# Kernel tuning notes

Measured on AMD Instinct MI355X. Metric: run time of the kernel, lower is better.

Reference implementation:

```python
import jax, jax.numpy as jnp
import numpy as np

B = 8192        # number of drug-cell pairs (graphs)
NPG = 32        # nodes per graph
EPG = 64        # directed edges per graph
N = B * NPG     # total nodes
E = B * EPG     # total edges
CELL = 908      # cell_inp_dim
BN_EPS = 1e-5


def _bn(x):
    # BatchNorm1d in training mode with gamma=1, beta=0 (fresh init), biased var
    m = x.mean(0)
    v = x.var(0)
    return (x - m) * jax.lax.rsqrt(v + BN_EPS)


def _lin_params(k, fan_in, fan_out):
    kw, _ = jax.random.split(k)
    w = jax.random.normal(kw, (fan_in, fan_out), jnp.float32) / np.sqrt(fan_in)
    b = jnp.zeros((fan_out,), jnp.float32)
    return w, b


_DIMS = [("ce_1", CELL, 516), ("ce_2", 516, 256), ("ce_3", 256, 128),
         ("g1_1", 9, 128), ("g1_2", 128, 128),
         ("g2_1", 128, 128), ("g2_2", 128, 128),
         ("d_1", 128, 128), ("d_2", 128, 128),
         ("f_1", 256, 128), ("f_2", 128, 64), ("f_3", 64, 1)]


def setup_inputs() -> dict:
    key = jax.random.key(0)
    ks = jax.random.split(key, 4 + len(_DIMS))
    inp = {}
    inp["cell"] = jax.random.normal(ks[0], (B, CELL), jnp.float32)
    inp["drug_x"] = jax.random.normal(ks[1], (N, 9), jnp.float32)
    g = jnp.arange(E) // EPG  # graph id per edge
    src = g * NPG + jax.random.randint(ks[2], (E,), 0, NPG)
    dst = g * NPG + jax.random.randint(ks[3], (E,), 0, NPG)
    inp["drug_edge_index"] = jnp.stack([src, dst]).astype(jnp.int32)
    inp["drug_batch"] = (jnp.arange(N) // NPG).astype(jnp.int32)
    for i, (nm, a, b) in enumerate(_DIMS):
        w, bb = _lin_params(ks[4 + i], a, b)
        inp[nm + "_w"] = w
        inp[nm + "_b"] = bb
    return inp


def _forward(cell, drug_x, src, dst, batch,
             ce_1_w, ce_1_b, ce_2_w, ce_2_b, ce_3_w, ce_3_b,
             g1_1_w, g1_1_b, g1_2_w, g1_2_b,
             g2_1_w, g2_1_b, g2_2_w, g2_2_b,
             d_1_w, d_1_b, d_2_w, d_2_b,
             f_1_w, f_1_b, f_2_w, f_2_b, f_3_w, f_3_b):
    # cell_emb branch (dropout = identity in eval/reference)
    c = jax.nn.relu(_bn(cell @ ce_1_w + ce_1_b))
    c = jax.nn.relu(_bn(c @ ce_2_w + ce_2_b))
    c = jax.nn.relu(_bn(c @ ce_3_w + ce_3_b))

    # GINConv 1: h = MLP((1+eps)*x + sum_{j in N(i)} x_j), eps=0
    agg = jax.ops.segment_sum(drug_x[src], dst, num_segments=N)
    h = drug_x + agg
    h = jax.nn.relu(_bn(h @ g1_1_w + g1_1_b)) @ g1_2_w + g1_2_b  # inner MLP: Lin-BN-ReLU-Lin
    h = _bn(jax.nn.relu(h))  # outer ReLU then BN (per Sequential order)

    # GINConv 2
    agg = jax.ops.segment_sum(h[src], dst, num_segments=N)
    h = h + agg
    h = jax.nn.relu(_bn(h @ g2_1_w + g2_1_b)) @ g2_2_w + g2_2_b
    h = _bn(jax.nn.relu(h))

    # global max pool over nodes of each graph -> [B, 128]
    p = jax.ops.segment_max(h, batch, num_segments=B)

    d = jax.nn.relu(_bn(p @ d_1_w + d_1_b))
    d = jax.nn.relu(d @ d_2_w + d_2_b)

    z = jnp.concatenate([c, d], axis=-1)  # [B, 256]
    z = jax.nn.elu(_bn(z @ f_1_w + f_1_b))
    z = jax.nn.elu(_bn(z @ f_2_w + f_2_b))
    y = (z @ f_3_w + f_3_b).reshape(B)
    return y


def reference(cell, drug_x, drug_edge_index, drug_batch,
              ce_1_w, ce_1_b, ce_2_w, ce_2_b, ce_3_w, ce_3_b,
              g1_1_w, g1_1_b, g1_2_w, g1_2_b,
              g2_1_w, g2_1_b, g2_2_w, g2_2_b,
              d_1_w, d_1_b, d_2_w, d_2_b,
              f_1_w, f_1_b, f_2_w, f_2_b, f_3_w, f_3_b):
    src, dst = drug_edge_index[0], drug_edge_index[1]
    return _forward(cell, drug_x, src, dst, drug_batch,
                    ce_1_w, ce_1_b, ce_2_w, ce_2_b, ce_3_w, ce_3_b,
                    g1_1_w, g1_1_b, g1_2_w, g1_2_b,
                    g2_1_w, g2_1_b, g2_2_w, g2_2_b,
                    d_1_w, d_1_b, d_2_w, d_2_b,
                    f_1_w, f_1_b, f_2_w, f_2_b, f_3_w, f_3_b)
```

## Files before the change

kernel.cpp:

```cpp
#include <hip/hip_runtime.h>
#include <hip/hip_bf16.h>
#include <math.h>

#define BGRAPH 8192
#define NPG 32
#define EPG 64
#define NNODE (BGRAPH * NPG)
#define NEDGE (BGRAPH * EPG)
#define CELLD 908
#define BN_EPS 1e-5f
#define ABF_STR 1024
#define C1_STR 640
#define HBS 136

typedef __attribute__((ext_vector_type(8))) short bf16x8;
typedef __attribute__((ext_vector_type(4))) float f32x4;
typedef __attribute__((ext_vector_type(4))) unsigned short us4;
typedef __attribute__((ext_vector_type(8))) unsigned short us8;

__device__ __forceinline__ unsigned short f2bf(float f)
{
    unsigned int u = __float_as_uint(f);
    u = (u + 0x7FFFu + ((u >> 16) & 1u)) >> 16;
    return (unsigned short)u;
}

__device__ __forceinline__ bf16x8 quant8(const float v[8])
{
    union { bf16x8 b; unsigned short u[8]; } fr;
    #pragma unroll
    for (int j = 0; j < 8; ++j) fr.u[j] = f2bf(v[j]);
    return fr.b;
}

__device__ __forceinline__ void bf2f8(bf16x8 b, float v[8])
{
    union { bf16x8 bb; unsigned short u[8]; } x; x.bb = b;
    #pragma unroll
    for (int j = 0; j < 8; ++j) v[j] = __uint_as_float((unsigned)x.u[j] << 16);
}

__device__ __forceinline__ float apply_in(float v, int mode, float mn, float iv)
{
    if (mode == 1)      { v = (v - mn) * iv; v = fmaxf(v, 0.f); }
    else if (mode == 2) { v = (v - mn) * iv; v = (v > 0.f) ? v : expm1f(v); }
    else if (mode == 3) { v = fmaxf(v, 0.f); v = (v - mn) * iv; }
    return v;
}

struct TransArgs {
    const float* w[11];
    unsigned short* wt[11];
    int K[11], N[11], ntN[11];
    int off[12];
};
struct TransSmem { float t[64][65]; };

__device__ void dev_transpose(TransSmem* sm, int b, const TransArgs& a)
{
    int tid = threadIdx.x;
    int s = 0;
    while (s < 10 && b >= a.off[s + 1]) ++s;
    int t0 = b - a.off[s];
    int K = a.K[s], N = a.N[s], ntn = a.ntN[s];
    int kt = t0 / ntn, nt = t0 - kt * ntn;
    int k0 = kt * 64, n0 = nt * 64;
    const float* w = a.w[s];
    unsigned short* wt = a.wt[s];
    int c = tid & 63, rg = tid >> 6;
    #pragma unroll
    for (int i = 0; i < 16; ++i) {
        int rr = rg * 16 + i;
        int k = k0 + rr, n = n0 + c;
        sm->t[c][rr] = (k < K && n < N) ? w[(size_t)k * N + n] : 0.f;
    }
    __syncthreads();
    #pragma unroll
    for (int i = 0; i < 16; ++i) {
        int rr = rg * 16 + i;
        int n = n0 + rr, k = k0 + c;
        if (n < N && k < K) wt[(size_t)n * K + k] = f2bf(sm->t[rr][c]);
    }
}

struct SetupArgs {
    float* zb; int zTotal; int zBlocks;
    const int* src; const int* dst; int* row_start; int* col_idx;
};
struct SetupSmem { int cnt[4][32]; int fill[4][32]; int rsl[4][33]; };

__device__ void dev_setup(SetupSmem* sm, int b, const SetupArgs& a)
{
    int tid = threadIdx.x;
    if (b < a.zBlocks) {
        int i = b * 256 + tid;
        if (i < a.zTotal) a.zb[i] = 0.f;
        return;
    }
    b -= a.zBlocks;
    int gl = tid >> 6, e = tid & 63;
    int g = b * 4 + gl;
    if (e < 32) { sm->cnt[gl][e] = 0; sm->fill[gl][e] = 0; }
    __syncthreads();
    int s = a.src[g * EPG + e] - g * NPG;
    int d = a.dst[g * EPG + e] - g * NPG;
    atomicAdd(&sm->cnt[gl][d], 1);
    __syncthreads();
    if (e == 0) {
        int acc = 0;
        for (int i = 0; i < 32; ++i) { sm->rsl[gl][i] = acc; acc += sm->cnt[gl][i]; }
        sm->rsl[gl][32] = acc;
    }
    __syncthreads();
    int pos = sm->rsl[gl][d] + atomicAdd(&sm->fill[gl][d], 1);
    a.col_idx[g * EPG + pos] = s;
    if (e < 33) a.row_start[g * 33 + e] = sm->rsl[gl][e];
}

__device__ void dev_quant_cell(int bid, const float* __restrict__ cell,
                               unsigned short* __restrict__ abf)
{
    int i = bid * 256 + threadIdx.x;
    int row = i / (ABF_STR / 4), c4 = i - row * (ABF_STR / 4);
    int k = c4 * 4;
    us4 w = (us4){0, 0, 0, 0};
    if (k < CELLD) {
        float4 f = *(const float4*)&cell[(size_t)row * CELLD + k];
        w = (us4){ f2bf(f.x), f2bf(f.y), f2bf(f.z), f2bf(f.w) };
    }
    *(us4*)&abf[(size_t)row * ABF_STR + k] = w;
}

__device__ void dev_quant_c1(int bid, const float* __restrict__ c1,
                             const float* __restrict__ stats, float inv_sM,
                             unsigned short* __restrict__ out)
{
    int i = bid * 256 + threadIdx.x;
    int row = i / (C1_STR / 4), c4 = i - row * (C1_STR / 4);
    int k = c4 * 4;
    us4 w = (us4){0, 0, 0, 0};
    if (k < 516) {
        float4 f = *(const float4*)&c1[(size_t)row * 516 + k];
        float v[4] = {f.x, f.y, f.z, f.w};
        #pragma unroll
        for (int j = 0; j < 4; ++j) {
            float s = stats[k + j], ss = stats[516 + k + j];
            float mn = s * inv_sM;
            float iv = rsqrtf(ss * inv_sM - mn * mn + BN_EPS);
            v[j] = fmaxf((v[j] - mn) * iv, 0.f);
        }
        w = (us4){ f2bf(v[0]), f2bf(v[1]), f2bf(v[2]), f2bf(v[3]) };
    }
    *(us4*)&out[(size_t)row * C1_STR + k] = w;
}

__device__ void dev_reduce(int bid, const float* __restrict__ part, int nrows,
                           int nt, float* __restrict__ out)
{
    int c = threadIdx.x;
    int per = nrows >> 6;
    int r0 = bid * per;
    bool isq = (c >= 128);
    int cc = isq ? c - 128 : c;
    if (cc >= nt) return;
    float s = 0.f;
    for (int r = 0; r < per; ++r) s += part[(size_t)(r0 + r) * 256 + c];
    unsafeAtomicAdd(&out[(isq ? nt : 0) + cc], s);
}

struct S1Smem {
    unsigned short h[4 * 32 * HBS];
    unsigned char ubuf[4096];
    int rs[4][36];
    int ci[4][64];
};

__device__ void dev_gin_s1(S1Smem* sm, int bid,
                           const float* __restrict__ drug_x,
                           const int* __restrict__ row_start,
                           const int* __restrict__ col_idx,
                           const unsigned short* __restrict__ W11,
                           const float* __restrict__ b11,
                           unsigned short* uout, float* __restrict__ part)
{
    unsigned short* w11l = (unsigned short*)sm->ubuf;
    float* red = (float*)sm->ubuf;

    int tid  = threadIdx.x;
    int wave = tid >> 6;
    int lane = tid & 63;
    int quad = lane >> 4;
    int l16  = lane & 15;
    int g0   = bid * 4;
    unsigned short* hw = sm->h + wave * (32 * HBS);
    float* xw = (float*)hw;

    for (int i = tid; i < 128 * 16; i += 256) {
        int n = i >> 4, k = i & 15;
        w11l[i] = (k < 9) ? W11[n * 9 + k] : (unsigned short)0;
    }
    if (tid < 132) {
        int gl = tid / 33, idx = tid - gl * 33;
        sm->rs[gl][idx] = row_start[(g0 + gl) * 33 + idx];
    }
    {
        int gl = tid >> 6, e = tid & 63;
        sm->ci[gl][e] = col_idx[(g0 + gl) * EPG + e];
    }
    {
        const float* xg = drug_x + (size_t)(g0 + wave) * 32 * 9;
        for (int i = lane; i < 32 * 16; i += 64) {
            int rr = i >> 4, c = i & 15;
            xw[i] = (c < 9) ? xg[rr * 9 + c] : 0.f;
        }
    }
    __syncthreads();

    f32x4 acc[2][8];
    #pragma unroll
    for (int i = 0; i < 2; ++i)
        #pragma unroll
        for (int j = 0; j < 8; ++j)
            acc[i][j] = (f32x4){0.f, 0.f, 0.f, 0.f};

    {
        bf16x8 af[2];
        #pragma unroll
        for (int mt = 0; mt < 2; ++mt) {
            int rowl = mt * 16 + l16;
            float v[8] = {0, 0, 0, 0, 0, 0, 0, 0};
            if (quad < 2) {
                float4 lo = *(const float4*)&xw[rowl * 16 + quad * 8];
                float4 hi = *(const float4*)&xw[rowl * 16 + quad * 8 + 4];
                v[0] = lo.x; v[1] = lo.y; v[2] = lo.z; v[3] = lo.w;
                v[4] = hi.x; v[5] = hi.y; v[6] = hi.z; v[7] = hi.w;
                int e0 = sm->rs[wave][rowl], e1 = sm->rs[wave][rowl + 1];
                for (int e = e0; e < e1; ++e) {
                    int sr = sm->ci[wave][e];
                    float4 l2 = *(const float4*)&xw[sr * 16 + quad * 8];
                    float4 h2 = *(const float4*)&xw[sr * 16 + quad * 8 + 4];
                    v[0] += l2.x; v[1] += l2.y; v[2] += l2.z; v[3] += l2.w;
                    v[4] += h2.x; v[5] += h2.y; v[6] += h2.z; v[7] += h2.w;
                }
            }
            af[mt] = quant8(v);
        }
        #pragma unroll
        for (int nt = 0; nt < 8; ++nt) {
            bf16x8 b;
            if (quad < 2) b = *(const bf16x8*)(const void*)&w11l[(nt * 16 + l16) * 16 + quad * 8];
            else { float z[8] = {0,0,0,0,0,0,0,0}; b = quant8(z); }
            acc[0][nt] = __builtin_amdgcn_mfma_f32_16x16x32_bf16(af[0], b, acc[0][nt], 0, 0, 0);
            acc[1][nt] = __builtin_amdgcn_mfma_f32_16x16x32_bf16(af[1], b, acc[1][nt], 0, 0, 0);
        }
    }

    float ls[8], lq[8];
    unsigned short* ub = uout + (size_t)(g0 + wave) * 32 * 128;
    #pragma unroll
    for (int nt = 0; nt < 8; ++nt) {
        int col = nt * 16 + l16;
        float bv = b11[col];
        float s0 = 0.f, q0 = 0.f;
        #pragma unroll
        for (int mt = 0; mt < 2; ++mt) {
            int rb = mt * 16 + quad * 4;
            #pragma unroll
            for (int r = 0; r < 4; ++r) {
                float u = acc[mt][nt][r] + bv;
                ub[(size_t)(rb + r) * 128 + col] = f2bf(u);
                s0 += u; q0 += u * u;
            }
        }
        ls[nt] = s0; lq[nt] = q0;
    }
    __syncthreads();
    #pragma unroll
    for (int nt = 0; nt < 8; ++nt) {
        float s = ls[nt], q = lq[nt];
        s += __shfl_xor(s, 16); q += __shfl_xor(q, 16);
        s += __shfl_xor(s, 32); q += __shfl_xor(q, 32);
        if (quad == 0) {
            int col = nt * 16 + l16;
            red[(wave * 2 + 0) * 128 + col] = s;
            red[(wave * 2 + 1) * 128 + col] = q;
        }
    }
    __syncthreads();
    if (tid < 128) {
        float s = red[0 * 128 + tid] + red[2 * 128 + tid] + red[4 * 128 + tid] + red[6 * 128 + tid];
        float q = red[1 * 128 + tid] + red[3 * 128 + tid] + red[5 * 128 + tid] + red[7 * 128 + tid];
        part[(size_t)bid * 256 + tid] = s;
        part[(size_t)bid * 256 + 128 + tid] = q;
    }
}

struct S3fSmem {
    unsigned short wsl[128 * 136];
    float pmv[256];
    int rs[2][33];
    int ci[2][64];
};

__device__ void dev_gin_s3f(S3fSmem* sm, int bid,
                            const unsigned short* __restrict__ uin,
                            const int* __restrict__ row_start,
                            const int* __restrict__ col_idx,
                            const unsigned short* __restrict__ Wt,
                            const float* __restrict__ bias,
                            const float* __restrict__ in_stats, float inv_sM,
                            unsigned short* __restrict__ uout,
                            float* __restrict__ part)
{
    float* zt = (float*)sm->wsl;

    int tid  = threadIdx.x;
    int wave = tid >> 6;
    int lane = tid & 63;
    int quad = lane >> 4;
    int l16  = lane & 15;
    int g0   = bid * 2;
    int row0 = bid * 64;

    if (tid < 128) {
        float s = in_stats[tid], ss = in_stats[128 + tid];
        float mn = s * inv_sM;
        sm->pmv[tid] = mn;
        sm->pmv[128 + tid] = rsqrtf(ss * inv_sM - mn * mn + BN_EPS);
    }
    if (tid < 66) {
        int gl = tid / 33, idx = tid - gl * 33;
        sm->rs[gl][idx] = row_start[(g0 + gl) * 33 + idx];
    }
    if (tid >= 128) {
        int t = tid - 128;
        sm->ci[t >> 6][t & 63] = col_idx[(g0 + (t >> 6)) * EPG + (t & 63)];
    }
    for (int i = tid; i < 128 * 32; i += 256) {
        int n = i >> 5, k = (i & 31) * 4;
        *(us4*)&sm->wsl[n * 136 + k] = *(const us4*)&Wt[(size_t)n * 128 + k];
    }
    __syncthreads();

    bf16x8 afrag[4];
    {
        const unsigned short* ap = uin + (size_t)(row0 + wave * 16 + l16) * 128;
        #pragma unroll
        for (int ks = 0; ks < 4; ++ks) {
            int kb = ks * 32 + quad * 8;
            float v[8];
            bf2f8(*(const bf16x8*)(const void*)&ap[kb], v);
            #pragma unroll
            for (int j = 0; j < 8; ++j)
                v[j] = (fmaxf(v[j], 0.f) - sm->pmv[kb + j]) * sm->pmv[128 + kb + j];
            afrag[ks] = quant8(v);
        }
    }

    f32x4 acc[8];
    #pragma unroll
    for (int j = 0; j < 8; ++j) acc[j] = (f32x4){0.f, 0.f, 0.f, 0.f};
    #pragma unroll
    for (int ks = 0; ks < 4; ++ks) {
        int kb = ks * 32 + quad * 8;
        #pragma unroll
        for (int nt = 0; nt < 8; ++nt) {
            bf16x8 b = *(const bf16x8*)(const void*)&sm->wsl[(nt * 16 + l16) * 136 + kb];
            acc[nt] = __builtin_amdgcn_mfma_f32_16x16x32_bf16(afrag[ks], b, acc[nt], 0, 0, 0);
        }
    }
    __syncthreads();

    #pragma unroll
    for (int nt = 0; nt < 8; ++nt) {
        int col = nt * 16 + l16;
        #pragma unroll
        for (int r = 0; r < 4; ++r)
            zt[(wave * 16 + quad * 4 + r) * 132 + col] = acc[nt][r];
    }
    __syncthreads();

    float sv[4] = {0.f, 0.f, 0.f, 0.f}, qv[4] = {0.f, 0.f, 0.f, 0.f};
    {
        int c4  = (tid & 31) * 4;
        int rg  = tid >> 5;
        int hh  = rg >> 2;
        int rb0 = (rg & 3) * 8;
        float4 bv = *(const float4*)&bias[c4];
        unsigned short* ub = uout + (size_t)row0 * 128;
        for (int rr = 0; rr < 8; ++rr) {
            int r = rb0 + rr;
            int lr = hh * 32 + r;
            float4 val = *(const float4*)&zt[lr * 132 + c4];
            int e0 = sm->rs[hh][r], e1 = sm->rs[hh][r + 1];
            for (int e = e0; e < e1; ++e) {
                float4 zz = *(const float4*)&zt[(hh * 32 + sm->ci[hh][e]) * 132 + c4];
                val.x += zz.x; val.y += zz.y; val.z += zz.z; val.w += zz.w;
            }
            float u0 = val.x + bv.x, u1 = val.y + bv.y;
            float u2 = val.z + bv.z, u3 = val.w + bv.w;
            *(us4*)&ub[(size_t)lr * 128 + c4] =
                (us4){ f2bf(u0), f2bf(u1), f2bf(u2), f2bf(u3) };
            sv[0] += u0; sv[1] += u1; sv[2] += u2; sv[3] += u3;
            qv[0] += u0 * u0; qv[1] += u1 * u1; qv[2] += u2 * u2; qv[3] += u3 * u3;
        }
    }
    __syncthreads();
    {
        int c4 = (tid & 31) * 4, rg = tid >> 5;
        #pragma unroll
        for (int j = 0; j < 4; ++j) {
            zt[rg * 128 + c4 + j] = sv[j];
            zt[1024 + rg * 128 + c4 + j] = qv[j];
        }
    }
    __syncthreads();
    if (tid < 128) {
        float s = 0.f, q = 0.f;
        #pragma unroll
        for (int rg = 0; rg < 8; ++rg) {
            s += zt[rg * 128 + tid];
            q += zt[1024 + rg * 128 + tid];
        }
        part[(size_t)bid * 256 + tid] = s;
        part[(size_t)bid * 256 + 128 + tid] = q;
    }
}

struct LinSmem {
    unsigned short Ws_l[128 * 136];
    float pmv[256];
    float red[4][2][128];
};

template<int DO_POOL>
__device__ void dev_gin_lin(LinSmem* sm, int bid,
                            const unsigned short* __restrict__ uin,
                            const unsigned short* __restrict__ Wt,
                            const float* __restrict__ bias,
                            const float* __restrict__ in_stats, float inv_sM,
                            unsigned short* uout,
                            float* __restrict__ part,
                            float* __restrict__ pool_out)
{
    int tid  = threadIdx.x;
    int wave = tid >> 6;
    int lane = tid & 63;
    int quad = lane >> 4;
    int l16  = lane & 15;
    int row0 = bid * 64;

    for (int i = tid; i < 128 * 32; i += 256) {
        int n = i >> 5, k = (i & 31) * 4;
        *(us4*)&sm->Ws_l[n * 136 + k] = *(const us4*)&Wt[(size_t)n * 128 + k];
    }
    if (tid < 128) {
        float s = in_stats[tid], ss = in_stats[128 + tid];
        float mn = s * inv_sM;
        sm->pmv[tid] = mn;
        sm->pmv[128 + tid] = rsqrtf(ss * inv_sM - mn * mn + BN_EPS);
    }
    __syncthreads();

    bf16x8 afrag[4];
    {
        const unsigned short* ap = uin + (size_t)(row0 + wave * 16 + l16) * 128;
        #pragma unroll
        for (int ks = 0; ks < 4; ++ks) {
            int kb = ks * 32 + quad * 8;
            float v[8];
            bf2f8(*(const bf16x8*)(const void*)&ap[kb], v);
            #pragma unroll
            for (int j = 0; j < 8; ++j)
                v[j] = fmaxf((v[j] - sm->pmv[kb + j]) * sm->pmv[128 + kb + j], 0.f);
            afrag[ks] = quant8(v);
        }
    }

    f32x4 acc[8];
    #pragma unroll
    for (int j = 0; j < 8; ++j) acc[j] = (f32x4){0.f, 0.f, 0.f, 0.f};
    #pragma unroll
    for (int ks = 0; ks < 4; ++ks) {
        int kb = ks * 32 + quad * 8;
        #pragma unroll
        for (int nt = 0; nt < 8; ++nt) {
            bf16x8 b = *(const bf16x8*)(const void*)&sm->Ws_l[(nt * 16 + l16) * 136 + kb];
            acc[nt] = __builtin_amdgcn_mfma_f32_16x16x32_bf16(afrag[ks], b, acc[nt], 0, 0, 0);
        }
    }

    float ls[8], lq[8], lm[8];
    #pragma unroll
    for (int nt = 0; nt < 8; ++nt) {
        int col = nt * 16 + l16;
        float bv = bias[col];
        int rb = row0 + wave * 16 + quad * 4;
        float s0 = 0.f, q0 = 0.f, mx = -INFINITY;
        #pragma unroll
        for (int r = 0; r < 4; ++r) {
            float u = acc[nt][r] + bv;
            float ru = fmaxf(u, 0.f);
            s0 += ru; q0 += ru * ru;
            if (DO_POOL) mx = fmaxf(mx, ru);
            else uout[(size_t)(rb + r) * 128 + col] = f2bf(u);
        }
        ls[nt] = s0; lq[nt] = q0; lm[nt] = mx;
    }

    #pragma unroll
    for (int nt = 0; nt < 8; ++nt) {
        float s = ls[nt], q = lq[nt];
        s += __shfl_xor(s, 16); q += __shfl_xor(q, 16);
        s += __shfl_xor(s, 32); q += __shfl_xor(q, 32);
        if (quad == 0) {
            sm->red[wave][0][nt * 16 + l16] = s;
            sm->red[wave][1][nt * 16 + l16] = q;
        }
    }
    __syncthreads();
    if (tid < 128) {
        float s = sm->red[0][0][tid] + sm->red[1][0][tid] + sm->red[2][0][tid] + sm->red[3][0][tid];
        float q = sm->red[0][1][tid] + sm->red[1][1][tid] + sm->red[2][1][tid] + sm->red[3][1][tid];
        part[(size_t)bid * 256 + tid] = s;
        part[(size_t)bid * 256 + 128 + tid] = q;
    }
    if (DO_POOL) {
        __syncthreads();
        #pragma unroll
        for (int nt = 0; nt < 8; ++nt) {
            float m = lm[nt];
            m = fmaxf(m, __shfl_xor(m, 16));
            m = fmaxf(m, __shfl_xor(m, 32));
            if (quad == 0) sm->red[wave][0][nt * 16 + l16] = m;
        }
        __syncthreads();
        {
            int gi = tid >> 7, col = tid & 127;
            float m = fmaxf(sm->red[gi * 2][0][col], sm->red[gi * 2 + 1][0][col]);
            pool_out[(size_t)((row0 >> 5) + gi) * 128 + col] = m;
        }
    }
}

struct RBSmem { float pm[256]; float pv[256]; };

template<int KSTEPS, int NT>
__device__ void dev_rB(RBSmem* sm, int bid,
                       const float* __restrict__ A, const float* __restrict__ A2,
                       int lda, int K, int stats_K, int ksplit,
                       const unsigned short* __restrict__ Wt,
                       const float* __restrict__ bias, float* __restrict__ C,
                       const float* __restrict__ in_stats, float inv_sM, int in_mode,
                       float* __restrict__ part, int stats_mode, int out_act)
{
    constexpr int NSUBW = NT / 64;
    int tid  = threadIdx.x;
    int wave = tid >> 6;
    int lane = tid & 63;
    int quad = lane >> 4;
    int l16  = lane & 15;
    int m0   = bid * 16;

    if (in_mode) {
        for (int k = tid; k < KSTEPS * 32; k += 256) {
            float mn = 0.f, iv = 1.f;
            if (k < stats_K) {
                float s = in_stats[k], ss = in_stats[stats_K + k];
                mn = s * inv_sM;
                float vr = ss * inv_sM - mn * mn;
                iv = rsqrtf(vr + BN_EPS);
            }
            sm->pm[k] = mn; sm->pv[k] = iv;
        }
        __syncthreads();
    }

    bf16x8 afrag[KSTEPS];
    {
        int row = m0 + l16;
        const float* ap = A + (size_t)row * lda;
        #pragma unroll
        for (int ks = 0; ks < KSTEPS; ++ks) {
            int kb = ks * 32 + quad * 8;
            float v[8];
            #pragma unroll
            for (int hh = 0; hh < 2; ++hh) {
                int k = kb + hh * 4;
                const float* p = (k >= ksplit) ? &A2[(size_t)row * 128 + (k - 128)]
                                               : &ap[k];
                float4 f = *(const float4*)p;
                v[hh * 4 + 0] = f.x; v[hh * 4 + 1] = f.y;
                v[hh * 4 + 2] = f.z; v[hh * 4 + 3] = f.w;
            }
            if (in_mode) {
                #pragma unroll
                for (int j = 0; j < 8; ++j)
                    v[j] = apply_in(v[j], in_mode, sm->pm[kb + j], sm->pv[kb + j]);
            }
            afrag[ks] = quant8(v);
        }
    }

    f32x4 acc[NSUBW];
    #pragma unroll
    for (int j = 0; j < NSUBW; ++j) acc[j] = (f32x4){0.f, 0.f, 0.f, 0.f};

    #pragma unroll
    for (int ks = 0; ks < KSTEPS; ++ks) {
        #pragma unroll
        for (int nt = 0; nt < NSUBW; ++nt) {
            int wrow = (wave * NSUBW + nt) * 16 + l16;
            bf16x8 b = *(const bf16x8*)(const void*)&Wt[(size_t)wrow * K + ks * 32 + quad * 8];
            acc[nt] = __builtin_amdgcn_mfma_f32_16x16x32_bf16(afrag[ks], b, acc[nt], 0, 0, 0);
        }
    }

    float ls[NSUBW], lq[NSUBW];
    #pragma unroll
    for (int nt = 0; nt < NSUBW; ++nt) { ls[nt] = 0.f; lq[nt] = 0.f; }

    #pragma unroll
    for (int nt = 0; nt < NSUBW; ++nt) {
        int col = (wave * NSUBW + nt) * 16 + l16;
        float bv = bias[col];
        int rbase = m0 + quad * 4;
        #pragma unroll
        for (int r = 0; r < 4; ++r) {
            float u = acc[nt][r] + bv;
            if (C) {
                float wv = out_act ? fmaxf(u, 0.f) : u;
                C[(size_t)(rbase + r) * NT + col] = wv;
            }
            if (stats_mode) {
                float s = (stats_mode == 2) ? fmaxf(u, 0.f) : u;
                ls[nt] += s; lq[nt] += s * s;
            }
        }
    }

    if (stats_mode) {
        #pragma unroll
        for (int nt = 0; nt < NSUBW; ++nt) {
            float s = ls[nt], q = lq[nt];
            s += __shfl_xor(s, 16); q += __shfl_xor(q, 16);
            s += __shfl_xor(s, 32); q += __shfl_xor(q, 32);
            if (quad == 0) {
                int col = (wave * NSUBW + nt) * 16 + l16;
                part[(size_t)bid * 256 + col] = s;
                part[(size_t)bid * 256 + 128 + col] = q;
            }
        }
    }
}

template<int NT>
struct CellSmem {
    unsigned short As_l[32 * 136];
    unsigned short Ws_l[NT * 136];
    float red[2][2][NT];
};

template<int NT>
__device__ void dev_gemm_cell(CellSmem<NT>* sm, int bid,
                              const unsigned short* __restrict__ Abf, int abf_str,
                              const unsigned short* __restrict__ Wt,
                              const float* __restrict__ bias, float* __restrict__ C,
                              int K, int N, float* __restrict__ out_stats)
{
    constexpr int NSUB = NT / 32;
    constexpr int WITEMS = NT * 32 / 256;
    int tid = threadIdx.x;
    int wave = tid >> 6;
    int lane = tid & 63;
    int quad = lane >> 4;
    int l16 = lane & 15;
    int mhalf = wave & 1, nhalf = wave >> 1;
    int m0 = (bid & 255) * 32, n0 = (bid >> 8) * NT;

    us8 aReg[2];
    us4 wReg[WITEMS];

    auto loadA = [&](int k0) {
        #pragma unroll
        for (int t = 0; t < 2; ++t) {
            int i = t * 256 + tid;
            int row = i >> 4, c8 = (i & 15) * 8;
            aReg[t] = *(const us8*)&Abf[(size_t)(m0 + row) * abf_str + k0 + c8];
        }
    };
    auto loadW = [&](int k0) {
        #pragma unroll
        for (int t = 0; t < WITEMS; ++t) {
            int i = t * 256 + tid;
            int nn = i >> 5, kt = i & 31;
            int k = k0 + kt * 4;
            int gn = n0 + nn;
            us4 w4 = (us4){0, 0, 0, 0};
            if (gn < N && k < K) w4 = *(const us4*)&Wt[(size_t)gn * K + k];
            wReg[t] = w4;
        }
    };
    auto storeAW = [&]() {
        #pragma unroll
        for (int t = 0; t < 2; ++t) {
            int i = t * 256 + tid;
            int row = i >> 4, c8 = (i & 15) * 8;
            *(us8*)&sm->As_l[row * 136 + c8] = aReg[t];
        }
        #pragma unroll
        for (int t = 0; t < WITEMS; ++t) {
            int i = t * 256 + tid;
            int nn = i >> 5, kt = i & 31;
            *(us4*)&sm->Ws_l[nn * 136 + kt * 4] = wReg[t];
        }
    };

    f32x4 acc[NSUB];
    #pragma unroll
    for (int j = 0; j < NSUB; ++j) acc[j] = (f32x4){0.f, 0.f, 0.f, 0.f};

    int nch = (K + 127) >> 7;
    loadA(0); loadW(0);
    for (int c = 0; c < nch; ++c) {
        storeAW();
        if (c + 1 < nch) { loadA((c + 1) * 128); loadW((c + 1) * 128); }
        __syncthreads();
        #pragma unroll
        for (int ks = 0; ks < 4; ++ks) {
            bf16x8 a = *(const bf16x8*)(const void*)
                &sm->As_l[(mhalf * 16 + l16) * 136 + ks * 32 + quad * 8];
            #pragma unroll
            for (int nt = 0; nt < NSUB; ++nt) {
                bf16x8 b = *(const bf16x8*)(const void*)
                    &sm->Ws_l[(nhalf * (NT / 2) + nt * 16 + l16) * 136 + ks * 32 + quad * 8];
                acc[nt] = __builtin_amdgcn_mfma_f32_16x16x32_bf16(a, b, acc[nt], 0, 0, 0);
            }
        }
        __syncthreads();
    }

    float ls[NSUB], lq[NSUB];
    #pragma unroll
    for (int nt = 0; nt < NSUB; ++nt) { ls[nt] = 0.f; lq[nt] = 0.f; }

    #pragma unroll
    for (int nt = 0; nt < NSUB; ++nt) {
        int col = n0 + nhalf * (NT / 2) + nt * 16 + l16;
        if (col < N) {
            float bv = bias[col];
            int rbase = m0 + mhalf * 16 + quad * 4;
            #pragma unroll
            for (int r = 0; r < 4; ++r) {
                float u = acc[nt][r] + bv;
                C[(size_t)(rbase + r) * N + col] = u;
                ls[nt] += u; lq[nt] += u * u;
            }
        }
    }

    #pragma unroll
    for (int nt = 0; nt < NSUB; ++nt) {
        float s = ls[nt], q = lq[nt];
        s += __shfl_xor(s, 16); q += __shfl_xor(q, 16);
        s += __shfl_xor(s, 32); q += __shfl_xor(q, 32);
        if (quad == 0) {
            int lc = nhalf * (NT / 2) + nt * 16 + l16;
            sm->red[mhalf][0][lc] = s;
            sm->red[mhalf][1][lc] = q;
        }
    }
    __syncthreads();
    if (tid < NT) {
        int col = n0 + tid;
        if (col < N) {
            float s = sm->red[0][0][tid] + sm->red[1][0][tid];
            float q = sm->red[0][1][tid] + sm->red[1][1][tid];
            unsafeAtomicAdd(&out_stats[col], s);
            unsafeAtomicAdd(&out_stats[N + col], q);
        }
    }
}

__global__ __launch_bounds__(256)
void prep(TransArgs ta, SetupArgs sa, const float* cell, unsigned short* abf,
          int nbT, int nbZC)
{
    __shared__ __align__(16) char smem[sizeof(TransSmem)];
    int b = blockIdx.x;
    if (b < nbT) { dev_transpose((TransSmem*)smem, b, ta); return; }
    b -= nbT;
    if (b < nbZC) { dev_setup((SetupSmem*)smem, b, sa); return; }
    b -= nbZC;
    dev_quant_cell(b, cell, abf);
}

__global__ __launch_bounds__(256)
void f_s1_ce1(const float* drug_x, const int* row_start, const int* col_idx,
              const unsigned short* W11, const float* b11,
              unsigned short* uout, float* partA,
              const unsigned short* Abf, const unsigned short* Wt0,
              const float* ce1b, float* c1, float* st_c1, int nb1)
{
    constexpr size_t SZ = sizeof(S1Smem) > sizeof(CellSmem<128>)
                        ? sizeof(S1Smem) : sizeof(CellSmem<128>);
    __shared__ __align__(16) char smem[SZ];
    int b = blockIdx.x;
    if (b < nb1)
        dev_gin_s1((S1Smem*)smem, b, drug_x, row_start, col_idx, W11, b11, uout, partA);
    else
        dev_gemm_cell<128>((CellSmem<128>*)smem, b - nb1, Abf, ABF_STR, Wt0,
                           ce1b, c1, CELLD, 516, st_c1);
}

__global__ __launch_bounds__(256)
void f_red_qc1(const float* partA, int nrows, float* out,
               const float* c1, const float* st_c1, float inv_B,
               unsigned short* c1bf, int nb1)
{
    int b = blockIdx.x;
    if (b < nb1) dev_reduce(b, partA, nrows, 128, out);
    else dev_quant_c1(b - nb1, c1, st_c1, inv_B, c1bf);
}

__global__ __launch_bounds__(256)
void f_lin0_ce2(const unsigned short* uin, const unsigned short* Wt4,
                const float* g12b, const float* st_u1, float inv_N,
                unsigned short* uout, float* partA,
                const unsigned short* C1bf, const unsigned short* Wt1,
                const float* ce2b, float* c2, float* st_c2, int nb1)
{
    constexpr size_t SZ = sizeof(LinSmem) > sizeof(CellSmem<64>)
                        ? sizeof(LinSmem) : sizeof(CellSmem<64>);
    __shared__ __align__(16) char smem[SZ];
    int b = blockIdx.x;
    if (b < nb1)
        dev_gin_lin<0>((LinSmem*)smem, b, uin, Wt4, g12b, st_u1, inv_N,
                       uout, partA, nullptr);
    else
        dev_gemm_cell<64>((CellSmem<64>*)smem, b - nb1, C1bf, C1_STR, Wt1,
                          ce2b, c2, 516, 256, st_c2);
}

__global__ __launch_bounds__(256)
void f_red_ce3(const float* partA, int nrows, float* out,
               const float* c2, const unsigned short* Wt2, const float* ce3b,
               float* c3u, const float* st_c2, float inv_B, float* partB, int nb1)
{
    __shared__ __align__(16) char smem[sizeof(RBSmem)];
    int b = blockIdx.x;
    if (b < nb1) dev_reduce(b, partA, nrows, 128, out);
    else dev_rB<8, 128>((RBSmem*)smem, b - nb1, c2, nullptr, 256, 256, 256,
                        1 << 30, Wt2, ce3b, c3u, st_c2, inv_B, 1, partB, 1, 0);
}

__global__ __launch_bounds__(256)
void f_s3f_red(const unsigned short* uin, const int* row_start, const int* col_idx,
               const unsigned short* Wt5, const float* g21b,
               const float* st_u2rel, float inv_N, unsigned short* uout,
               float* partA, const float* partB, int nrowsB, float* st_c3, int nb1)
{
    __shared__ __align__(16) char smem[sizeof(S3fSmem)];
    int b = blockIdx.x;
    if (b < nb1)
        dev_gin_s3f((S3fSmem*)smem, b, uin, row_start, col_idx, Wt5, g21b,
                    st_u2rel, inv_N, uout, partA);
    else
        dev_reduce(b - nb1, partB, nrowsB, 128, st_c3);
}

__global__ __launch_bounds__(256)
void reduce_stats(const float* __restrict__ part, int nrows, int nt,
                  float* __restrict__ out)
{
    dev_reduce(blockIdx.x, part, nrows, nt, out);
}

__global__ __launch_bounds__(256)
void gin_lin1(const unsigned short* uin, const unsigned short* Wt,
              const float* bias, const float* in_stats, float inv_sM,
              float* part, float* pool_out)
{
    __shared__ __align__(16) char smem[sizeof(LinSmem)];
    dev_gin_lin<1>((LinSmem*)smem, blockIdx.x, uin, Wt, bias, in_stats, inv_sM,
                   nullptr, part, pool_out);
}

template<int KSTEPS, int NT>
__global__ __launch_bounds__(256)
void gemm_rB(const float* A, const float* A2, int lda, int K, int stats_K,
             int ksplit, const unsigned short* Wt, const float* bias, float* C,
             const float* in_stats, float inv_sM, int in_mode,
             float* part, int stats_mode, int out_act)
{
    __shared__ __align__(16) char smem[sizeof(RBSmem)];
    dev_rB<KSTEPS, NT>((RBSmem*)smem, blockIdx.x, A, A2, lda, K, stats_K, ksplit,
                       Wt, bias, C, in_stats, inv_sM, in_mode, part, stats_mode, out_act);
}

__global__ void final_dot(const float* __restrict__ u, const float* __restrict__ w,
                          const float* __restrict__ b, float* __restrict__ y,
                          const float* __restrict__ stats, float inv_sM)
{
    __shared__ float pmv[64], piv[64], sw[64];
    int tid = threadIdx.x;
    if (tid < 64) {
        float s = stats[tid], ss = stats[64 + tid];
        float mn = s * inv_sM;
        float vr = ss * inv_sM - mn * mn;
        pmv[tid] = mn;
        piv[tid] = rsqrtf(vr + BN_EPS);
        sw[tid] = w[tid];
    }
    __syncthreads();
    int i = blockIdx.x * blockDim.x + tid;
    if (i >= BGRAPH) return;
    float acc = 0.f;
    #pragma unroll
    for (int k = 0; k < 64; ++k) {
        float v = (u[(size_t)i * 64 + k] - pmv[k]) * piv[k];
        v = (v > 0.f) ? v : expm1f(v);
        acc += v * sw[k];
    }
    y[i] = acc + b[0];
}

extern "C" void kernel_launch(void* const* d_in, const int* in_sizes, int n_in,
                              void* d_out, int out_size, void* d_ws, size_t ws_size,
                              hipStream_t stream)
{
    const float* cell   = (const float*)d_in[0];
    const float* drug_x = (const float*)d_in[1];
    const int*   eidx   = (const int*)d_in[2];
    const float* ce1w = (const float*)d_in[4];  const float* ce1b = (const float*)d_in[5];
    const float* ce2w = (const float*)d_in[6];  const float* ce2b = (const float*)d_in[7];
    const float* ce3w = (const float*)d_in[8];  const float* ce3b = (const float*)d_in[9];
    const float* g11w = (const float*)d_in[10]; const float* g11b = (const float*)d_in[11];
    const float* g12w = (const float*)d_in[12]; const float* g12b = (const float*)d_in[13];
    const float* g21w = (const float*)d_in[14]; const float* g21b = (const float*)d_in[15];
    const float* g22w = (const float*)d_in[16]; const float* g22b = (const float*)d_in[17];
    const float* d1w  = (const float*)d_in[18]; const float* d1b  = (const float*)d_in[19];
    const float* d2w  = (const float*)d_in[20]; const float* d2b  = (const float*)d_in[21];
    const float* f1w  = (const float*)d_in[22]; const float* f1b  = (const float*)d_in[23];
    const float* f2w  = (const float*)d_in[24]; const float* f2b  = (const float*)d_in[25];
    const float* f3w  = (const float*)d_in[26]; const float* f3b  = (const float*)d_in[27];

    const int* src = eidx;
    const int* dst = eidx + NEDGE;
    float* out = (float*)d_out;

    const float INV_N = 1.f / (float)NNODE;
    const float INV_B = 1.f / (float)BGRAPH;
    const int KBIG = 1 << 30;

    float* ws = (float*)d_ws;
    unsigned short* ubg = (unsigned short*)ws;
    float* pbuf = ws + (size_t)NNODE * 64;
    float* sb   = pbuf + (size_t)BGRAPH * 128;
    unsigned short* wtb = (unsigned short*)(sb + 10 * 1032);
    auto ST = [&](int i) { return sb + (size_t)i * 1032; };
    float* st_u1    = ST(0);
    float* st_u2rel = ST(1);
    float* st_u3    = ST(2);
    float* st_u4rel = ST(3);
    float* st_c1    = ST(4);
    float* st_c2    = ST(5);
    float* st_c3    = ST(6);
    float* st_d1    = ST(7);
    float* st_f1    = ST(8);
    float* st_f2    = ST(9);

    struct WDef { const float* w; int K; int N; };
    WDef wd[11] = {
        {ce1w, CELLD, 516}, {ce2w, 516, 256}, {ce3w, 256, 128},
        {g11w, 9, 128}, {g12w, 128, 128}, {g21w, 128, 128}, {g22w, 128, 128},
        {d1w, 128, 128}, {d2w, 128, 128}, {f1w, 256, 128}, {f2w, 128, 64}
    };
    TransArgs ta;
    int off = 0;
    unsigned short* wt[11];
    ta.off[0] = 0;
    for (int i = 0; i < 11; ++i) {
        wt[i] = wtb + off;
        ta.w[i] = wd[i].w; ta.wt[i] = wt[i];
        ta.K[i] = wd[i].K; ta.N[i] = wd[i].N;
        ta.ntN[i] = (wd[i].N + 63) / 64;
        ta.off[i + 1] = ta.off[i] + ((wd[i].K + 63) / 64) * ta.ntN[i];
        off += wd[i].K * wd[i].N;
    }

    SetupArgs sa;
    sa.zb = sb; sa.zTotal = 10 * 1032; sa.zBlocks = (10 * 1032 + 255) / 256;
    sa.src = src; sa.dst = dst;

    int csr_off = (off + 7) & ~7;
    int* row_start = (int*)(wtb + csr_off);
    int* col_idx   = row_start + (size_t)BGRAPH * 33;
    float* partA = (float*)(col_idx + (size_t)NEDGE);
    float* partB = partA + (size_t)4096 * 256;
    unsigned short* Abf  = (unsigned short*)(partB + (size_t)512 * 256);
    unsigned short* C1bf = Abf + (size_t)BGRAPH * ABF_STR;
    float* cellws = (float*)(C1bf + (size_t)BGRAPH * C1_STR);
    float* c1  = cellws;
    float* c2  = cellws;
    float* c3u = cellws + (size_t)BGRAPH * 256;
    float* dbuf  = ws;
    float* d2buf = dbuf + (size_t)BGRAPH * 128;
    float* f1o   = d2buf + (size_t)BGRAPH * 128;
    float* f2o   = f1o + (size_t)BGRAPH * 128;
    sa.row_start = row_start; sa.col_idx = col_idx;

    int nbT = ta.off[11];
    int nbZC = sa.zBlocks + BGRAPH / 4;

    prep<<<nbT + nbZC + 8192, 256, 0, stream>>>(ta, sa, cell, Abf, nbT, nbZC);

    f_s1_ce1<<<2048 + 1280, 256, 0, stream>>>(
        drug_x, row_start, col_idx, wt[3], g11b, ubg, partA,
        Abf, wt[0], ce1b, c1, st_c1, 2048);

    f_red_qc1<<<64 + 5120, 256, 0, stream>>>(
        partA, BGRAPH / 4, st_u1, c1, st_c1, INV_B, C1bf, 64);

    f_lin0_ce2<<<4096 + 1024, 256, 0, stream>>>(
        ubg, wt[4], g12b, st_u1, INV_N, ubg, partA,
        C1bf, wt[1], ce2b, c2, st_c2, 4096);

    f_red_ce3<<<64 + 512, 256, 0, stream>>>(
        partA, NNODE / 64, st_u2rel, c2, wt[2], ce3b, c3u, st_c2, INV_B, partB, 64);

    f_s3f_red<<<4096 + 64, 256, 0, stream>>>(
        ubg, row_start, col_idx, wt[5], g21b, st_u2rel, INV_N, ubg, partA,
        partB, BGRAPH / 16, st_c3, 4096);

    reduce_stats<<<64, 256, 0, stream>>>(partA, BGRAPH / 2, 128, st_u3);

    gin_lin1<<<NNODE / 64, 256, 0, stream>>>(
        ubg, wt[6], g22b, st_u3, INV_N, partA, pbuf);
    reduce_stats<<<64, 256, 0, stream>>>(partA, NNODE / 64, 128, st_u4rel);

    gemm_rB<4, 128><<<BGRAPH / 16, 256, 0, stream>>>(
        pbuf, nullptr, 128, 128, 128, KBIG, wt[7], d1b, dbuf,
        st_u4rel, INV_N, 3, partA, 1, 0);
    reduce_stats<<<64, 256, 0, stream>>>(partA, BGRAPH / 16, 128, st_d1);
    gemm_rB<4, 128><<<BGRAPH / 16, 256, 0, stream>>>(
        dbuf, nullptr, 128, 128, 128, KBIG, wt[8], d2b, d2buf,
        st_d1, INV_B, 1, partA, 0, 1);

    gemm_rB<8, 128><<<BGRAPH / 16, 256, 0, stream>>>(
        c3u, d2buf, 128, 256, 128, 128, wt[9], f1b, f1o,
        st_c3, INV_B, 1, partA, 1, 0);
    reduce_stats<<<64, 256, 0, stream>>>(partA, BGRAPH / 16, 128, st_f1);
    gemm_rB<4, 64><<<BGRAPH / 16, 256, 0, stream>>>(
        f1o, nullptr, 128, 128, 128, KBIG, wt[10], f2b, f2o,
        st_f1, INV_B, 2, partA, 1, 0);
    reduce_stats<<<64, 256, 0, stream>>>(partA, BGRAPH / 16, 64, st_f2);
    final_dot<<<BGRAPH / 256, 256, 0, stream>>>(f2o, f3w, f3b, out, st_f2, INV_B);
}
```

Measured before the change: 517.1 us.

## Re-pair cell MLP stages with later GIN stages in fused launches

Changes how the cell-embedding GEMM stages are co-scheduled with the GIN stages. ce1 now runs alongside lin0, ce2 alongside s3f, and ce3 alongside lin1, and the two remaining stat reductions are merged into one launch. GIN stage 1 now runs alone in its own kernel with a separate reduce, and its shared-memory struct shrinks to just the float staging buffer, which could raise occupancy. The aim is to balance the heavy cell GEMMs against the heavier GIN stages so each fused launch has more even work. It keeps the launch count about the same, since one launch is added and another removed.

```diff
diff --git a/kernel.cpp b/kernel.cpp
--- a/kernel.cpp
+++ b/kernel.cpp
@@ -11,7 +11,6 @@
 #define BN_EPS 1e-5f
 #define ABF_STR 1024
 #define C1_STR 640
-#define HBS 136
 
 typedef __attribute__((ext_vector_type(8))) short bf16x8;
 typedef __attribute__((ext_vector_type(4))) float f32x4;
@@ -169,7 +168,7 @@
 }
 
 struct S1Smem {
-    unsigned short h[4 * 32 * HBS];
+    float xw[4][32 * 16];
     unsigned char ubuf[4096];
     int rs[4][36];
     int ci[4][64];
@@ -192,8 +191,7 @@
     int quad = lane >> 4;
     int l16  = lane & 15;
     int g0   = bid * 4;
-    unsigned short* hw = sm->h + wave * (32 * HBS);
-    float* xw = (float*)hw;
+    float* xw = sm->xw[wave];
 
     for (int i = tid; i < 128 * 16; i += 256) {
         int n = i >> 4, k = i & 15;
@@ -796,77 +794,90 @@
 }
 
 __global__ __launch_bounds__(256)
-void f_s1_ce1(const float* drug_x, const int* row_start, const int* col_idx,
+void gin_s1_k(const float* drug_x, const int* row_start, const int* col_idx,
               const unsigned short* W11, const float* b11,
-              unsigned short* uout, float* partA,
-              const unsigned short* Abf, const unsigned short* Wt0,
-              const float* ce1b, float* c1, float* st_c1, int nb1)
-{
-    constexpr size_t SZ = sizeof(S1Smem) > sizeof(CellSmem<128>)
-                        ? sizeof(S1Smem) : sizeof(CellSmem<128>);
-    __shared__ __align__(16) char smem[SZ];
-    int b = blockIdx.x;
-    if (b < nb1)
-        dev_gin_s1((S1Smem*)smem, b, drug_x, row_start, col_idx, W11, b11, uout, partA);
-    else
-        dev_gemm_cell<128>((CellSmem<128>*)smem, b - nb1, Abf, ABF_STR, Wt0,
-                           ce1b, c1, CELLD, 516, st_c1);
+              unsigned short* uout, float* partA)
+{
+    __shared__ __align__(16) char smem[sizeof(S1Smem)];
+    dev_gin_s1((S1Smem*)smem, blockIdx.x, drug_x, row_start, col_idx,
+               W11, b11, uout, partA);
 }
 
 __global__ __launch_bounds__(256)
-void f_red_qc1(const float* partA, int nrows, float* out,
-               const float* c1, const float* st_c1, float inv_B,
-               unsigned short* c1bf, int nb1)
-{
-    int b = blockIdx.x;
-    if (b < nb1) dev_reduce(b, partA, nrows, 128, out);
-    else dev_quant_c1(b - nb1, c1, st_c1, inv_B, c1bf);
-}
-
-__global__ __launch_bounds__(256)
-void f_lin0_ce2(const unsigned short* uin, const unsigned short* Wt4,
+void f_lin0_ce1(const unsigned short* uin, const unsigned short* Wt4,
                 const float* g12b, const float* st_u1, float inv_N,
                 unsigned short* uout, float* partA,
-                const unsigned short* C1bf, const unsigned short* Wt1,
-                const float* ce2b, float* c2, float* st_c2, int nb1)
-{
-    constexpr size_t SZ = sizeof(LinSmem) > sizeof(CellSmem<64>)
-                        ? sizeof(LinSmem) : sizeof(CellSmem<64>);
+                const unsigned short* Abf, const unsigned short* Wt0,
+                const float* ce1b, float* c1, float* st_c1, int nb1)
+{
+    constexpr size_t SZ = sizeof(LinSmem) > sizeof(CellSmem<128>)
+                        ? sizeof(LinSmem) : sizeof(CellSmem<128>);
     __shared__ __align__(16) char smem[SZ];
     int b = blockIdx.x;
     if (b < nb1)
         dev_gin_lin<0>((LinSmem*)smem, b, uin, Wt4, g12b, st_u1, inv_N,
                        uout, partA, nullptr);
     else
-        dev_gemm_cell<64>((CellSmem<64>*)smem, b - nb1, C1bf, C1_STR, Wt1,
-                          ce2b, c2, 516, 256, st_c2);
+        dev_gemm_cell<128>((CellSmem<128>*)smem, b - nb1, Abf, ABF_STR, Wt0,
+                           ce1b, c1, CELLD, 516, st_c1);
 }
 
 __global__ __launch_bounds__(256)
-void f_red_ce3(const float* partA, int nrows, float* out,
-               const float* c2, const unsigned short* Wt2, const float* ce3b,
-               float* c3u, const float* st_c2, float inv_B, float* partB, int nb1)
-{
-    __shared__ __align__(16) char smem[sizeof(RBSmem)];
+void f_red_qc1(const float* partA, int nrows, float* out,
+               const float* c1, const float* st_c1, float inv_B,
+               unsigned short* c1bf, int nb1)
+{
     int b = blockIdx.x;
     if (b < nb1) dev_reduce(b, partA, nrows, 128, out);
-    else dev_rB<8, 128>((RBSmem*)smem, b - nb1, c2, nullptr, 256, 256, 256,
-                        1 << 30, Wt2, ce3b, c3u, st_c2, inv_B, 1, partB, 1, 0);
+    else dev_quant_c1(b - nb1, c1, st_c1, inv_B, c1bf);
 }
 
 __global__ __launch_bounds__(256)
-void f_s3f_red(const unsigned short* uin, const int* row_start, const int* col_idx,
+void f_s3f_ce2(const unsigned short* uin, const int* row_start, const int* col_idx,
                const unsigned short* Wt5, const float* g21b,
                const float* st_u2rel, float inv_N, unsigned short* uout,
-               float* partA, const float* partB, int nrowsB, float* st_c3, int nb1)
-{
-    __shared__ __align__(16) char smem[sizeof(S3fSmem)];
+               float* partA,
+               const unsigned short* C1bf, const unsigned short* Wt1,
+               const float* ce2b, float* c2, float* st_c2, int nb1)
+{
+    constexpr size_t SZ = sizeof(S3fSmem) > sizeof(CellSmem<64>)
+                        ? sizeof(S3fSmem) : sizeof(CellSmem<64>);
+    __shared__ __align__(16) char smem[SZ];
     int b = blockIdx.x;
     if (b < nb1)
         dev_gin_s3f((S3fSmem*)smem, b, uin, row_start, col_idx, Wt5, g21b,
                     st_u2rel, inv_N, uout, partA);
     else
-        dev_reduce(b - nb1, partB, nrowsB, 128, st_c3);
+        dev_gemm_cell<64>((CellSmem<64>*)smem, b - nb1, C1bf, C1_STR, Wt1,
+                          ce2b, c2, 516, 256, st_c2);
+}
+
+__global__ __launch_bounds__(256)
+void f_lin1_ce3(const unsigned short* uin, const unsigned short* Wt6,
+                const float* g22b, const float* st_u3, float inv_N,
+                float* partA, float* pool_out,
+                const float* c2, const unsigned short* Wt2, const float* ce3b,
+                float* c3u, const float* st_c2, float inv_B, float* partB, int nb1)
+{
+    constexpr size_t SZ = sizeof(LinSmem) > sizeof(RBSmem)
+                        ? sizeof(LinSmem) : sizeof(RBSmem);
+    __shared__ __align__(16) char smem[SZ];
+    int b = blockIdx.x;
+    if (b < nb1)
+        dev_gin_lin<1>((LinSmem*)smem, b, uin, Wt6, g22b, st_u3, inv_N,
+                       nullptr, partA, pool_out);
+    else
+        dev_rB<8, 128>((RBSmem*)smem, b - nb1, c2, nullptr, 256, 256, 256,
+                       1 << 30, Wt2, ce3b, c3u, st_c2, inv_B, 1, partB, 1, 0);
+}
+
+__global__ __launch_bounds__(256)
+void f_red2(const float* partA, int nrowsA, float* outA,
+            const float* partB, int nrowsB, float* outB)
+{
+    int b = blockIdx.x;
+    if (b < 64) dev_reduce(b, partA, nrowsA, 128, outA);
+    else dev_reduce(b - 64, partB, nrowsB, 128, outB);
 }
 
 __global__ __launch_bounds__(256)
@@ -874,16 +885,6 @@
                   float* __restrict__ out)
 {
     dev_reduce(blockIdx.x, part, nrows, nt, out);
-}
-
-__global__ __launch_bounds__(256)
-void gin_lin1(const unsigned short* uin, const unsigned short* Wt,
-              const float* bias, const float* in_stats, float inv_sM,
-              float* part, float* pool_out)
-{
-    __shared__ __align__(16) char smem[sizeof(LinSmem)];
-    dev_gin_lin<1>((LinSmem*)smem, blockIdx.x, uin, Wt, bias, in_stats, inv_sM,
-                   nullptr, part, pool_out);
 }
 
 template<int KSTEPS, int NT>
@@ -1015,29 +1016,30 @@
 
     prep<<<nbT + nbZC + 8192, 256, 0, stream>>>(ta, sa, cell, Abf, nbT, nbZC);
 
-    f_s1_ce1<<<2048 + 1280, 256, 0, stream>>>(
-        drug_x, row_start, col_idx, wt[3], g11b, ubg, partA,
-        Abf, wt[0], ce1b, c1, st_c1, 2048);
+    gin_s1_k<<<BGRAPH / 4, 256, 0, stream>>>(
+        drug_x, row_start, col_idx, wt[3], g11b, ubg, partA);
+
+    reduce_stats<<<64, 256, 0, stream>>>(partA, BGRAPH / 4, 128, st_u1);
+
+    f_lin0_ce1<<<4096 + 1280, 256, 0, stream>>>(
+        ubg, wt[4], g12b, st_u1, INV_N, ubg, partA,
+        Abf, wt[0], ce1b, c1, st_c1, 4096);
 
     f_red_qc1<<<64 + 5120, 256, 0, stream>>>(
-        partA, BGRAPH / 4, st_u1, c1, st_c1, INV_B, C1bf, 64);
-
-    f_lin0_ce2<<<4096 + 1024, 256, 0, stream>>>(
-        ubg, wt[4], g12b, st_u1, INV_N, ubg, partA,
+        partA, NNODE / 64, st_u2rel, c1, st_c1, INV_B, C1bf, 64);
+
+    f_s3f_ce2<<<4096 + 1024, 256, 0, stream>>>(
+        ubg, row_start, col_idx, wt[5], g21b, st_u2rel, INV_N, ubg, partA,
         C1bf, wt[1], ce2b, c2, st_c2, 4096);
 
-    f_red_ce3<<<64 + 512, 256, 0, stream>>>(
-        partA, NNODE / 64, st_u2rel, c2, wt[2], ce3b, c3u, st_c2, INV_B, partB, 64);
-
-    f_s3f_red<<<4096 + 64, 256, 0, stream>>>(
-        ubg, row_start, col_idx, wt[5], g21b, st_u2rel, INV_N, ubg, partA,
-        partB, BGRAPH / 16, st_c3, 4096);
-
     reduce_stats<<<64, 256, 0, stream>>>(partA, BGRAPH / 2, 128, st_u3);
 
-    gin_lin1<<<NNODE / 64, 256, 0, stream>>>(
-        ubg, wt[6], g22b, st_u3, INV_N, partA, pbuf);
-    reduce_stats<<<64, 256, 0, stream>>>(partA, NNODE / 64, 128, st_u4rel);
+    f_lin1_ce3<<<4096 + 512, 256, 0, stream>>>(
+        ubg, wt[6], g22b, st_u3, INV_N, partA, pbuf,
+        c2, wt[2], ce3b, c3u, st_c2, INV_B, partB, 4096);
+
+    f_red2<<<128, 256, 0, stream>>>(
+        partA, NNODE / 64, st_u4rel, partB, BGRAPH / 16, st_c3);
 
     gemm_rB<4, 128><<<BGRAPH / 16, 256, 0, stream>>>(
         pbuf, nullptr, 128, 128, 128, KBIG, wt[7], d1b, dbuf,
```

New measurement: 535.5 us. +3.6%, slower.
